# Kernel optimization log

Hardware: AMD Instinct MI355X
Metric: run time of the kernel (lower is better)

## Reference

```python
import jax, jax.numpy as jnp
import numpy as np

B = 8192       # Monte Carlo paths
NSTEP = 30     # Euler time steps
D = 100        # z_dim / number of assets
H1 = 110
H2 = 110
T = NSTEP - 1  # number of subnets
DT = np.float32(1.0 / NSTEP)
R = np.float32(0.05)   # riskfree
EPS = np.float32(1e-3) # Keras BatchNormalization epsilon


def setup_inputs() -> dict:
    key = jax.random.key(0)
    ks = jax.random.split(key, 25)
    f = jnp.float32
    X = jax.random.normal(ks[0], (B, NSTEP, D), f)
    DWs = jax.random.normal(ks[1], (B, NSTEP, D), f) * jnp.sqrt(DT)
    sigmas = jax.random.uniform(ks[2], (D,), f, 0.1, 0.4)
    y_init = jax.random.uniform(ks[3], (1,), f, 0.0, 1.0)
    z_init = jax.random.uniform(ks[4], (1, D), f, -0.1, 0.1)
    W1 = jax.random.normal(ks[5], (T, D, H1), f) / np.sqrt(D).astype(np.float32)
    W2 = jax.random.normal(ks[6], (T, H1, H2), f) / np.sqrt(H1).astype(np.float32)
    W3 = jax.random.normal(ks[7], (T, H2, D), f) / np.sqrt(H2).astype(np.float32)
    dims = [D, H1, H2, D]
    bn = {}
    for j, dim in enumerate(dims):
        bn[f"g{j}"] = 1.0 + 0.1 * jax.random.normal(ks[8 + 4 * j], (T, dim), f)
        bn[f"b{j}"] = 0.05 * jax.random.normal(ks[9 + 4 * j], (T, dim), f)
        bn[f"m{j}"] = 0.1 * jax.random.normal(ks[10 + 4 * j], (T, dim), f)
        bn[f"v{j}"] = jax.random.uniform(ks[11 + 4 * j], (T, dim), f, 0.5, 1.5)
    return dict(X=X, DWs=DWs, sigmas=sigmas, y_init=y_init, z_init=z_init,
                W1=W1, W2=W2, W3=W3, **bn)


def _bn(x, g, b, m, v):
    # Keras BatchNormalization, inference mode
    return (x - m) * jax.lax.rsqrt(v + EPS) * g + b


def _subnet(x, p):
    (w1, w2, w3, g0, b0, m0, v0, g1, b1, m1, v1,
     g2, b2, m2, v2, g3, b3, m3, v3) = p
    x = _bn(x, g0, b0, m0, v0)
    x = jax.nn.relu(x @ w1)
    x = _bn(x, g1, b1, m1, v1)
    x = jax.nn.relu(x @ w2)
    x = _bn(x, g2, b2, m2, v2)
    x = x @ w3
    return _bn(x, g3, b3, m3, v3)


def reference(X, DWs, sigmas, y_init, z_init, W1, W2, W3,
              g0, b0, m0, v0, g1, b1, m1, v1,
              g2, b2, m2, v2, g3, b3, m3, v3):
    nb = X.shape[0]
    Y0 = jnp.ones((nb, 1), X.dtype) * y_init            # [B,1]
    Z0 = jnp.ones((nb, 1), X.dtype) * z_init            # [B,D]

    def step(carry, xs):
        Y, Z = carry
        Xi, Xn, DWi, p = xs
        Y = Y + R * Y * DT + jnp.sum(sigmas * Xi * Z * DWi, axis=1, keepdims=True)
        Z = _subnet(Xn, p)
        return (Y, Z), None

    params = (W1, W2, W3, g0, b0, m0, v0, g1, b1, m1, v1,
              g2, b2, m2, v2, g3, b3, m3, v3)  # each leading dim T
    xs = (jnp.moveaxis(X[:, :T], 1, 0),        # [T,B,D]
          jnp.moveaxis(X[:, 1:T + 1], 1, 0),   # [T,B,D]
          jnp.moveaxis(DWs[:, :T], 1, 0),      # [T,B,D]
          params)
    (Y, Z), _ = jax.lax.scan(step, (Y0, Z0), xs)
    # final step: X[:,-2,:] with DWs[:,-1,:]
    Y = Y + R * Y * DT + jnp.sum(sigmas * X[:, -2, :] * Z * DWs[:, -1, :],
                                 axis=1, keepdims=True)
    return Y
```

## Files before the change

kernel.cpp:

```cpp
#include <hip/hip_runtime.h>

typedef unsigned short ushort_t;
typedef __attribute__((ext_vector_type(8))) short s16x8;
typedef __attribute__((ext_vector_type(4))) float f32x4;

#define B_PATHS 8192
#define NSTEP   30
#define DD      100
#define HH      110
#define TT      29
#define ROWSTR  3000
#define LDK     136
#define WFRAGSZ 14336
#define DT_C    (1.0f/30.0f)
#define R_C     0.05f
#define EPS_C   1e-3f

__device__ __forceinline__ ushort_t f2bf(float f) {
  unsigned u = __float_as_uint(f);
  u = u + 0x7FFFu + ((u >> 16) & 1u);
  return (ushort_t)(u >> 16);
}
__device__ __forceinline__ float bf2f(ushort_t u) {
  return __uint_as_float(((unsigned)u) << 16);
}

__global__ void prep_kernel(const float* __restrict__ W1, const float* __restrict__ W2,
                            const float* __restrict__ W3,
                            const float* g0, const float* b0, const float* m0, const float* v0,
                            const float* g1, const float* b1, const float* m1, const float* v1,
                            const float* g2, const float* b2, const float* m2, const float* v2,
                            const float* g3, const float* b3, const float* m3, const float* v3,
                            ushort_t* __restrict__ wprep, float* __restrict__ bprep)
{
  const int mat = blockIdx.x, t = blockIdx.y, tid = threadIdx.x;
  __shared__ float wsh[110*110];
  __shared__ float sin_[112], hin_[112], sout_[112], hout_[112];

  int Kr, Nr; const float* W; const float *g, *bb, *mm, *vv;
  if (mat == 0)      { Kr = 100; Nr = 110; W = W1 + t*11000; g = g0+t*100; bb = b0+t*100; mm = m0+t*100; vv = v0+t*100; }
  else if (mat == 1) { Kr = 110; Nr = 110; W = W2 + t*12100; g = g1+t*110; bb = b1+t*110; mm = m1+t*110; vv = v1+t*110; }
  else               { Kr = 110; Nr = 100; W = W3 + t*11000; g = g2+t*110; bb = b2+t*110; mm = m2+t*110; vv = v2+t*110; }

  if (tid < Kr) {
    float s = g[tid] * rsqrtf(vv[tid] + EPS_C);
    sin_[tid] = s; hin_[tid] = bb[tid] - mm[tid]*s;
  }
  if (mat == 2 && tid < Nr) {
    float s = g3[t*100+tid] * rsqrtf(v3[t*100+tid] + EPS_C);
    sout_[tid] = s; hout_[tid] = b3[t*100+tid] - m3[t*100+tid]*s;
  }
  for (int i = tid; i < Kr*Nr; i += 256) wsh[i] = W[i];
  __syncthreads();

  if (tid < 128) {
    float c = 0.f;
    if (tid < Nr) {
      for (int k = 0; k < Kr; ++k) c += hin_[k] * wsh[k*Nr + tid];
      if (mat == 2) c = c * sout_[tid] + hout_[tid];
    }
    bprep[(t*3 + mat)*128 + tid] = c;
  }

  ushort_t* wo = wprep + (size_t)(t*3 + mat) * WFRAGSZ;
  for (int ch = tid; ch < 1792; ch += 256) {
    const int lane = ch & 63, ntkb = ch >> 6;
    const int nt = ntkb % 7, kb = ntkb / 7;
    const int n  = nt*16 + (lane & 15);
    const int k0 = kb*32 + (lane >> 4)*8;
    ushort_t tmp[8];
#pragma unroll
    for (int j = 0; j < 8; ++j) {
      const int k = k0 + j;
      float v = 0.f;
      if (n < Nr && k < Kr) {
        v = sin_[k] * wsh[k*Nr + n];
        if (mat == 2) v *= sout_[n];
      }
      tmp[j] = f2bf(v);
    }
    ushort4 lo; lo.x = tmp[0]; lo.y = tmp[1]; lo.z = tmp[2]; lo.w = tmp[3];
    ushort4 hi; hi.x = tmp[4]; hi.y = tmp[5]; hi.z = tmp[6]; hi.w = tmp[7];
    *(ushort4*)(wo + ch*8)     = lo;
    *(ushort4*)(wo + ch*8 + 4) = hi;
  }
}

__device__ __forceinline__ void mlp_stage(const ushort_t* actIn, const ushort_t* __restrict__ wfrag,
                                          const float* __restrict__ biasg, ushort_t* actOut,
                                          int wr, int lane, int lrow, int quad, bool relu)
{
  f32x4 acc[7];
  const f32x4 z4 = {0.f, 0.f, 0.f, 0.f};
#pragma unroll
  for (int nt = 0; nt < 7; ++nt) acc[nt] = z4;
  s16x8 a[4];
#pragma unroll
  for (int kb = 0; kb < 4; ++kb)
    a[kb] = *(const s16x8*)(actIn + (wr + lrow)*LDK + kb*32 + quad*8);
#pragma unroll
  for (int kb = 0; kb < 4; ++kb) {
#pragma unroll
    for (int nt = 0; nt < 7; ++nt) {
      s16x8 b = *(const s16x8*)(wfrag + ((kb*7 + nt)*64 + lane)*8);
      acc[nt] = __builtin_amdgcn_mfma_f32_16x16x32_bf16(a[kb], b, acc[nt], 0, 0, 0);
    }
  }
#pragma unroll
  for (int nt = 0; nt < 7; ++nt) {
    const int col = nt*16 + lrow;
    const float bv = biasg[col];
#pragma unroll
    for (int r = 0; r < 4; ++r) {
      float u = acc[nt][r] + bv;
      if (relu) u = u > 0.f ? u : 0.f;
      actOut[(wr + quad*4 + r)*LDK + col] = f2bf(u);
    }
  }
#pragma unroll
  for (int r = 0; r < 4; ++r)
    actOut[(wr + quad*4 + r)*LDK + 112 + lrow] = 0;
}

__global__ __launch_bounds__(256, 4)
void subnet_kernel(const float* __restrict__ X, const float* __restrict__ DW,
                   const float* __restrict__ sigmas,
                   const ushort_t* __restrict__ wprep, const float* __restrict__ bprep,
                   float* __restrict__ sbuf)
{
  __shared__ __align__(16) ushort_t actA[64*LDK];
  __shared__ __align__(16) ushort_t actB[64*LDK];

  const int tid  = threadIdx.x;
  const int t    = blockIdx.y;
  const int m0   = blockIdx.x * 64;
  const int lane = tid & 63, lrow = lane & 15, quad = lane >> 4;
  const int wr   = (tid >> 6) * 16;

  for (int j = tid; j < 64*32; j += 256) {
    const int r = j >> 5, c = j & 31;
    ushort4 u; u.x = 0; u.y = 0; u.z = 0; u.w = 0;
    if (c < 25) {
      const float4 v = *(const float4*)(X + (size_t)(m0 + r)*ROWSTR + (t+1)*DD + c*4);
      u.x = f2bf(v.x); u.y = f2bf(v.y); u.z = f2bf(v.z); u.w = f2bf(v.w);
    }
    *(ushort4*)(actA + r*LDK + c*4) = u;
  }
  __syncthreads();

  const ushort_t* wf = wprep + (size_t)(t*3) * WFRAGSZ;
  const float*    bg = bprep + (t*3) * 128;

  mlp_stage(actA, wf,             bg,       actB, wr, lane, lrow, quad, true);
  __syncthreads();
  mlp_stage(actB, wf + WFRAGSZ,   bg + 128, actA, wr, lane, lrow, quad, true);
  __syncthreads();
  mlp_stage(actA, wf + 2*WFRAGSZ, bg + 256, actB, wr, lane, lrow, quad, false);
  __syncthreads();

  {
    const int row = tid >> 2, part = tid & 3;
    const int b   = m0 + row;
    const int xt  = (t == TT - 1) ? (NSTEP - 2) : (t + 1);
    const float* xr = X  + (size_t)b*ROWSTR + xt*DD;
    const float* dr = DW + (size_t)b*ROWSTR + (t+1)*DD;
    float p = 0.f;
#pragma unroll
    for (int g = part; g < 25; g += 4) {
      const float4 xv = *(const float4*)(xr + g*4);
      const float4 dv = *(const float4*)(dr + g*4);
      const float4 sg = *(const float4*)(sigmas + g*4);
      const ushort4 zu = *(const ushort4*)(actB + row*LDK + g*4);
      p += sg.x*xv.x*dv.x*bf2f(zu.x);
      p += sg.y*xv.y*dv.y*bf2f(zu.y);
      p += sg.z*xv.z*dv.z*bf2f(zu.z);
      p += sg.w*xv.w*dv.w*bf2f(zu.w);
    }
    p += __shfl_xor(p, 1, 64);
    p += __shfl_xor(p, 2, 64);
    if (part == 0)
      sbuf[(size_t)(t+1)*B_PATHS + b] = p;
  }
}

__global__ void y_kernel(const float* __restrict__ X, const float* __restrict__ DW,
                         const float* __restrict__ sigmas, const float* __restrict__ y_init,
                         const float* __restrict__ z_init, const float* __restrict__ sbuf,
                         float* __restrict__ out)
{
  const int b = blockIdx.x * blockDim.x + threadIdx.x;
  const float* xr = X + (size_t)b * ROWSTR;
  const float* dr = DW + (size_t)b * ROWSTR;
  float s0 = 0.f;
#pragma unroll 5
  for (int c = 0; c < 25; ++c) {
    float4 xv = *(const float4*)(xr + c*4);
    float4 dv = *(const float4*)(dr + c*4);
    float4 sg = *(const float4*)(sigmas + c*4);
    float4 zv = *(const float4*)(z_init + c*4);
    s0 += sg.x*xv.x*zv.x*dv.x;
    s0 += sg.y*xv.y*zv.y*dv.y;
    s0 += sg.z*xv.z*zv.z*dv.z;
    s0 += sg.w*xv.w*zv.w*dv.w;
  }
  float y = y_init[0];
  y = y + R_C*y*DT_C + s0;
#pragma unroll
  for (int tau = 1; tau < NSTEP; ++tau)
    y = y + R_C*y*DT_C + sbuf[(size_t)tau*B_PATHS + b];
  out[b] = y;
}

extern "C" void kernel_launch(void* const* d_in, const int* in_sizes, int n_in,
                              void* d_out, int out_size, void* d_ws, size_t ws_size,
                              hipStream_t stream) {
  const float* X      = (const float*)d_in[0];
  const float* DWs    = (const float*)d_in[1];
  const float* sigmas = (const float*)d_in[2];
  const float* y_init = (const float*)d_in[3];
  const float* z_init = (const float*)d_in[4];
  const float* W1     = (const float*)d_in[5];
  const float* W2     = (const float*)d_in[6];
  const float* W3     = (const float*)d_in[7];
  const float* bn[16];
  for (int i = 0; i < 16; ++i) bn[i] = (const float*)d_in[8 + i];

  char* ws = (char*)d_ws;
  ushort_t* wprep = (ushort_t*)ws;
  float*    bprep = (float*)(ws + 2494464);
  float*    sbuf  = (float*)(ws + 2539008);
  float*    out   = (float*)d_out;

  prep_kernel<<<dim3(3, TT), 256, 0, stream>>>(
      W1, W2, W3,
      bn[0], bn[1], bn[2], bn[3],  bn[4], bn[5], bn[6], bn[7],
      bn[8], bn[9], bn[10], bn[11], bn[12], bn[13], bn[14], bn[15],
      wprep, bprep);
  subnet_kernel<<<dim3(B_PATHS/64, TT), 256, 0, stream>>>(
      X, DWs, sigmas, wprep, bprep, sbuf);
  y_kernel<<<dim3(B_PATHS/256), 256, 0, stream>>>(
      X, DWs, sigmas, y_init, z_init, sbuf, out);
}
```

Measured before the change: 335.8 us.

## Give each wavefront private LDS tiles and drop block barriers; prefetch DW early

Each of the four waves now owns its own 16-row activation buffers, so the three MLP stages need no block-wide __syncthreads; compiler memory barriers keep the intra-wave LDS ordering. The DW row slice for the final dot product is loaded into registers at kernel start, so its latency overlaps with the MLP. The cost is more live registers (28 floats), which may raise register pressure under the 4-waves launch bound, and correctness now relies on in-order LDS access within a wave.

```diff
diff --git a/kernel.cpp b/kernel.cpp
--- a/kernel.cpp
+++ b/kernel.cpp
@@ -88,7 +88,7 @@
 
 __device__ __forceinline__ void mlp_stage(const ushort_t* actIn, const ushort_t* __restrict__ wfrag,
                                           const float* __restrict__ biasg, ushort_t* actOut,
-                                          int wr, int lane, int lrow, int quad, bool relu)
+                                          int lane, int lrow, int quad, bool relu)
 {
   f32x4 acc[7];
   const f32x4 z4 = {0.f, 0.f, 0.f, 0.f};
@@ -97,7 +97,7 @@
   s16x8 a[4];
 #pragma unroll
   for (int kb = 0; kb < 4; ++kb)
-    a[kb] = *(const s16x8*)(actIn + (wr + lrow)*LDK + kb*32 + quad*8);
+    a[kb] = *(const s16x8*)(actIn + lrow*LDK + kb*32 + quad*8);
 #pragma unroll
   for (int kb = 0; kb < 4; ++kb) {
 #pragma unroll
@@ -106,6 +106,7 @@
       acc[nt] = __builtin_amdgcn_mfma_f32_16x16x32_bf16(a[kb], b, acc[nt], 0, 0, 0);
     }
   }
+  __asm__ volatile("" ::: "memory");
 #pragma unroll
   for (int nt = 0; nt < 7; ++nt) {
     const int col = nt*16 + lrow;
@@ -114,12 +115,13 @@
     for (int r = 0; r < 4; ++r) {
       float u = acc[nt][r] + bv;
       if (relu) u = u > 0.f ? u : 0.f;
-      actOut[(wr + quad*4 + r)*LDK + col] = f2bf(u);
+      actOut[(quad*4 + r)*LDK + col] = f2bf(u);
     }
   }
 #pragma unroll
   for (int r = 0; r < 4; ++r)
-    actOut[(wr + quad*4 + r)*LDK + 112 + lrow] = 0;
+    actOut[(quad*4 + r)*LDK + 112 + lrow] = 0;
+  __asm__ volatile("" ::: "memory");
 }
 
 __global__ __launch_bounds__(256, 4)
@@ -128,58 +130,70 @@
                    const ushort_t* __restrict__ wprep, const float* __restrict__ bprep,
                    float* __restrict__ sbuf)
 {
-  __shared__ __align__(16) ushort_t actA[64*LDK];
-  __shared__ __align__(16) ushort_t actB[64*LDK];
+  __shared__ __align__(16) ushort_t actA[4][16*LDK];
+  __shared__ __align__(16) ushort_t actB[4][16*LDK];
 
   const int tid  = threadIdx.x;
+  const int wv   = tid >> 6;
   const int t    = blockIdx.y;
-  const int m0   = blockIdx.x * 64;
+  const int m0   = blockIdx.x * 64 + wv * 16;
   const int lane = tid & 63, lrow = lane & 15, quad = lane >> 4;
-  const int wr   = (tid >> 6) * 16;
-
-  for (int j = tid; j < 64*32; j += 256) {
-    const int r = j >> 5, c = j & 31;
+  const int row16 = lane >> 2, part = lane & 3;
+  const int brow  = m0 + row16;
+
+  ushort_t* A  = actA[wv];
+  ushort_t* Bq = actB[wv];
+
+  const float* drp = DW + (size_t)brow*ROWSTR + (t+1)*DD;
+  float4 dwv[7];
+#pragma unroll
+  for (int g = 0; g < 7; ++g) {
+    const int c = part + g*4;
+    if (c < 25) dwv[g] = *(const float4*)(drp + c*4);
+    else        { dwv[g].x = 0.f; dwv[g].y = 0.f; dwv[g].z = 0.f; dwv[g].w = 0.f; }
+  }
+
+  const float* xrp = X + (size_t)brow*ROWSTR + (t+1)*DD;
+#pragma unroll
+  for (int g = 0; g < 8; ++g) {
+    const int c = part + g*4;
     ushort4 u; u.x = 0; u.y = 0; u.z = 0; u.w = 0;
     if (c < 25) {
-      const float4 v = *(const float4*)(X + (size_t)(m0 + r)*ROWSTR + (t+1)*DD + c*4);
+      const float4 v = *(const float4*)(xrp + c*4);
       u.x = f2bf(v.x); u.y = f2bf(v.y); u.z = f2bf(v.z); u.w = f2bf(v.w);
     }
-    *(ushort4*)(actA + r*LDK + c*4) = u;
-  }
-  __syncthreads();
+    *(ushort4*)(A + row16*LDK + c*4) = u;
+  }
+  __asm__ volatile("" ::: "memory");
 
   const ushort_t* wf = wprep + (size_t)(t*3) * WFRAGSZ;
   const float*    bg = bprep + (t*3) * 128;
 
-  mlp_stage(actA, wf,             bg,       actB, wr, lane, lrow, quad, true);
-  __syncthreads();
-  mlp_stage(actB, wf + WFRAGSZ,   bg + 128, actA, wr, lane, lrow, quad, true);
-  __syncthreads();
-  mlp_stage(actA, wf + 2*WFRAGSZ, bg + 256, actB, wr, lane, lrow, quad, false);
-  __syncthreads();
+  mlp_stage(A,  wf,             bg,       Bq, lane, lrow, quad, true);
+  mlp_stage(Bq, wf + WFRAGSZ,   bg + 128, A,  lane, lrow, quad, true);
+  mlp_stage(A,  wf + 2*WFRAGSZ, bg + 256, Bq, lane, lrow, quad, false);
 
   {
-    const int row = tid >> 2, part = tid & 3;
-    const int b   = m0 + row;
-    const int xt  = (t == TT - 1) ? (NSTEP - 2) : (t + 1);
-    const float* xr = X  + (size_t)b*ROWSTR + xt*DD;
-    const float* dr = DW + (size_t)b*ROWSTR + (t+1)*DD;
+    const int xt = (t == TT - 1) ? (NSTEP - 2) : (t + 1);
+    const float* xe = X + (size_t)brow*ROWSTR + xt*DD;
     float p = 0.f;
 #pragma unroll
-    for (int g = part; g < 25; g += 4) {
-      const float4 xv = *(const float4*)(xr + g*4);
-      const float4 dv = *(const float4*)(dr + g*4);
-      const float4 sg = *(const float4*)(sigmas + g*4);
-      const ushort4 zu = *(const ushort4*)(actB + row*LDK + g*4);
-      p += sg.x*xv.x*dv.x*bf2f(zu.x);
-      p += sg.y*xv.y*dv.y*bf2f(zu.y);
-      p += sg.z*xv.z*dv.z*bf2f(zu.z);
-      p += sg.w*xv.w*dv.w*bf2f(zu.w);
+    for (int g = 0; g < 7; ++g) {
+      const int c = part + g*4;
+      if (c < 25) {
+        const float4 xv = *(const float4*)(xe + c*4);
+        const float4 sg = *(const float4*)(sigmas + c*4);
+        const ushort4 zu = *(const ushort4*)(Bq + row16*LDK + c*4);
+        p += sg.x*xv.x*dwv[g].x*bf2f(zu.x);
+        p += sg.y*xv.y*dwv[g].y*bf2f(zu.y);
+        p += sg.z*xv.z*dwv[g].z*bf2f(zu.z);
+        p += sg.w*xv.w*dwv[g].w*bf2f(zu.w);
+      }
     }
     p += __shfl_xor(p, 1, 64);
     p += __shfl_xor(p, 2, 64);
     if (part == 0)
-      sbuf[(size_t)(t+1)*B_PATHS + b] = p;
+      sbuf[(size_t)(t+1)*B_PATHS + brow] = p;
   }
 }
 
```

Measured after the change: 336.7 us. Within noise of the previous version (+0.3%).
